# Performance work log

Hardware: AMD Instinct MI355X
Metric: run time of the kernel (lower is better)

## Reference

```python
import jax, jax.numpy as jnp
import numpy as np

START_TAG = 7
STOP_TAG = 8
NEG = -10000.0  # matches torch.full((1,K), -10000.) in the original


def setup_inputs() -> dict:
    key = jax.random.key(0)
    k1, k2, k3, k4 = jax.random.split(key, 4)
    B, T, K = 1024, 2048, 9  # K = output_dim + 2 (START/STOP hardcoded as 7/8)
    feats = jax.random.normal(k1, (B, T, K), dtype=jnp.float32)
    tags = jax.random.randint(k2, (B, T), 0, 7)            # valid labels 0..6
    lengths = jax.random.randint(k3, (B,), 1, T + 1)        # per-sentence lengths >= 1
    transitions = jax.random.normal(k4, (K, K), dtype=jnp.float32)
    transitions = transitions.at[START_TAG, :].set(NEG)     # never transition into START
    transitions = transitions.at[:, STOP_TAG].set(NEG)      # never transition out of STOP
    return {"feats": feats, "transitions": transitions, "tags": tags, "lengths": lengths}


def _crf_nll(feats, transitions, tags, lengths):
    # feats: [B,T,K] emissions, transitions[j,i] = score of i -> j
    B, T, K = feats.shape

    def fwd_one(feat, length):
        # CRF forward algorithm (log partition), vectorized over tags,
        # lax.scan over time; masked past `length` to emulate feats[:x_len].
        alpha0 = jnp.full((K,), NEG, feat.dtype).at[START_TAG].set(0.0)

        def step(alpha, inp):
            t, f = inp
            # alpha_new[j] = logsumexp_i(alpha[i] + transitions[j,i]) + feat[t,j]
            new = jax.nn.logsumexp(alpha[None, :] + transitions, axis=1) + f
            return jnp.where(t < length, new, alpha), None

        alpha, _ = jax.lax.scan(step, alpha0, (jnp.arange(T), feat))
        return jax.nn.logsumexp(alpha + transitions[STOP_TAG])

    fwd_scores = jax.vmap(fwd_one)(feats, lengths)  # [B]

    def gold_one(feat, tg, length):
        # _score_sentence: sum_t trans[tags[t], tags[t-1]] + feat[t, tags[t]]
        prev = jnp.concatenate([jnp.array([START_TAG], tg.dtype), tg[:-1]])
        step_scores = transitions[tg, prev] + jnp.take_along_axis(feat, tg[:, None], axis=1)[:, 0]
        mask = jnp.arange(tg.shape[0]) < length
        last = tg[length - 1]
        return jnp.sum(jnp.where(mask, step_scores, 0.0)) + transitions[STOP_TAG, last]

    gold_scores = jax.vmap(gold_one)(feats, tags, lengths)  # [B]

    # neg_log_likelihood accumulates (forward - gold) per sentence, then / n
    return jnp.mean(fwd_scores - gold_scores)


def reference(feats, transitions, tags, lengths):
    return _crf_nll(feats, transitions, tags, lengths)
```

## Files before the change

kernel.cpp:

```cpp
#include <hip/hip_runtime.h>


#define START_TAG 7
#define STOP_TAG  8
#define KDIM      9
#define NS        7
#define CHUNKS    32
#define NEGINF    (-1e30f)

__device__ __forceinline__ float rfl(float x) {
    return __int_as_float(__builtin_amdgcn_readfirstlane(__float_as_int(x)));
}

__global__ __launch_bounds__(256) void crf_fused_kernel(
    const float* __restrict__ feats,
    const float* __restrict__ trans,
    const int*   __restrict__ tags,
    const int*   __restrict__ lengths,
    float* __restrict__ out,
    int B, int T, int L)
{
    __shared__ float s_trans[81];
    __shared__ float s_E[49];
    __shared__ float s_M[CHUNKS * 64];
    __shared__ float s_gold[4];

    const int tid = threadIdx.x;
    const int b   = blockIdx.x;

    if (tid < 81) s_trans[tid] = trans[tid];
    if (tid >= 128 && tid < 177) {
        int k = tid - 128;
        s_E[k] = __expf(trans[(k / 7) * 9 + (k % 7)]);
    }
    __syncthreads();

    const int    len   = lengths[b];
    const int*   tg    = tags  + (size_t)b * T;
    const float* fbase = feats + (size_t)b * T * KDIM;

    {
        int per = (T >> 8) > 0 ? (T >> 8) : 1;
        int t0  = tid * per;
        float g = 0.f;
        if (t0 < len) {
            int te   = min(t0 + per, len);
            int prev = (t0 == 0) ? START_TAG : tg[t0 - 1];
            if (per == 8) {
                #pragma unroll
                for (int k = 0; k < 8; ++k) {
                    int t   = t0 + k;
                    int tc  = min(t, te - 1);
                    int cur = tg[tc];
                    float v = s_trans[cur * 9 + prev] + fbase[(size_t)tc * KDIM + cur];
                    g += (t < te) ? v : 0.f;
                    prev = cur;
                }
            } else {
                for (int k = 0; k < per; ++k) {
                    int t   = t0 + k;
                    int tc  = min(t, te - 1);
                    int cur = tg[tc];
                    float v = s_trans[cur * 9 + prev] + fbase[(size_t)tc * KDIM + cur];
                    g += (t < te) ? v : 0.f;
                    prev = cur;
                }
            }
            if (len - 1 >= t0 && len - 1 < t0 + per)
                g += s_trans[STOP_TAG * 9 + tg[len - 1]];
        }
        #pragma unroll
        for (int off = 32; off > 0; off >>= 1) g += __shfl_xor(g, off, 64);
        if ((tid & 63) == 0) s_gold[tid >> 6] = g;
    }

    {
        const int lane8  = tid & 7;
        const int c      = tid >> 3;
        const int t0     = c * L;
        const int tstart = max(t0, 1);
        const int tend   = min(t0 + L, len);

        if (lane8 < NS) {
            float* Mw = s_M + c * 64;
            if (tstart < tend) {
                float E[49];
                #pragma unroll
                for (int k = 0; k < 49; ++k) E[k] = rfl(s_E[k]);

                int baddr[NS];
                #pragma unroll
                for (int j = 0; j < NS; ++j) baddr[j] = (((tid & 56) | j) << 2);

                float p[NS];
                #pragma unroll
                for (int j = 0; j < NS; ++j) p[j] = (j == lane8) ? 1.f : 0.f;
                float s = 0.f;
                int rem = tend - tstart;

                const float* fp = fbase + (size_t)tstart * KDIM + lane8;

                #define CRF_STEP(XF) do {                                       \
                    float q[NS];                                                \
                    _Pragma("unroll")                                           \
                    for (int j = 0; j < NS; ++j) {                              \
                        float acc = E[j * 7] * p[0];                            \
                        _Pragma("unroll")                                       \
                        for (int i = 1; i < NS; ++i)                            \
                            acc = fmaf(E[j * 7 + i], p[i], acc);                \
                        q[j] = acc;                                             \
                    }                                                           \
                    float myef = __expf(XF);                                    \
                    _Pragma("unroll")                                           \
                    for (int j = 0; j < NS; ++j) {                              \
                        float efj = __int_as_float(                             \
                            __builtin_amdgcn_ds_bpermute(                       \
                                baddr[j], __float_as_int(myef)));               \
                        p[j] = q[j] * efj;                                      \
                    }                                                           \
                } while (0)

                #define CRF_RENORM() do {                                       \
                    float m = p[0];                                             \
                    _Pragma("unroll")                                           \
                    for (int j = 1; j < NS; ++j) m = fmaxf(m, p[j]);            \
                    float rm = __builtin_amdgcn_rcpf(m);                        \
                    _Pragma("unroll")                                           \
                    for (int j = 0; j < NS; ++j) p[j] *= rm;                    \
                    s += __logf(m);                                             \
                } while (0)

                int o1 = KDIM * min(1, rem - 1);
                int o2 = KDIM * min(2, rem - 1);
                int o3 = KDIM * min(3, rem - 1);
                float x0 = fp[0], x1 = fp[o1], x2 = fp[o2], x3 = fp[o3];
                fp += 4 * KDIM;

                while (rem >= 8) {
                    float y0 = fp[0], y1 = fp[KDIM], y2 = fp[2 * KDIM], y3 = fp[3 * KDIM];
                    fp += 4 * KDIM;
                    CRF_STEP(x0); CRF_STEP(x1); CRF_STEP(x2); CRF_STEP(x3);
                    CRF_RENORM();
                    x0 = y0; x1 = y1; x2 = y2; x3 = y3;
                    rem -= 4;
                }
                if (rem > 4) {
                    int e1 = KDIM * min(1, rem - 5);
                    int e2 = KDIM * min(2, rem - 5);
                    float y0 = fp[0], y1 = fp[e1], y2 = fp[e2];
                    CRF_STEP(x0); CRF_STEP(x1); CRF_STEP(x2); CRF_STEP(x3);
                    CRF_RENORM();
                    x0 = y0; x1 = y1; x2 = y2;
                    rem -= 4;
                }
                CRF_STEP(x0);
                if (rem > 1) CRF_STEP(x1);
                if (rem > 2) CRF_STEP(x2);
                if (rem > 3) CRF_STEP(x3);

                #pragma unroll
                for (int j = 0; j < NS; ++j)
                    Mw[j * 8 + lane8] = __logf(p[j]) + s;
                #undef CRF_STEP
                #undef CRF_RENORM
            } else {
                #pragma unroll
                for (int j = 0; j < NS; ++j)
                    Mw[j * 8 + lane8] = (j == lane8) ? 0.f : NEGINF;
            }
        }
    }
    __syncthreads();

    if (tid < 8) {
        const int  lane  = tid;
        const bool isrow = (lane < NS);
        const int  row   = isrow ? lane : 0;

        float a, S;
        {
            float a0 = isrow ? (s_trans[lane * 9 + START_TAG] + fbase[lane]) : NEGINF;
            float m = a0;
            #pragma unroll
            for (int off = 4; off > 0; off >>= 1) m = fmaxf(m, __shfl_xor(m, off, 8));
            a = a0 - m;
            S = m;
        }

        const int nc = min(CHUNKS, (len + L - 1) / L);
        const float* Mr0 = s_M + row * 8;
        float4 mA = *(const float4*)(Mr0);
        float4 mB = *(const float4*)(Mr0 + 4);
        for (int c = 0; c < nc; ++c) {
            int cn = min(c + 1, CHUNKS - 1);
            float4 nA = *(const float4*)(Mr0 + cn * 64);
            float4 nB = *(const float4*)(Mr0 + cn * 64 + 4);
            float tv[NS] = { mA.x, mA.y, mA.z, mA.w, mB.x, mB.y, mB.z };
            float tm = NEGINF;
            #pragma unroll
            for (int i = 0; i < NS; ++i) {
                tv[i] += __shfl(a, i, 8);
                tm = fmaxf(tm, tv[i]);
            }
            float sum = 0.f;
            #pragma unroll
            for (int i = 0; i < NS; ++i) sum += __expf(tv[i] - tm);
            float na = isrow ? (tm + __logf(sum)) : NEGINF;
            float m2 = na;
            #pragma unroll
            for (int off = 4; off > 0; off >>= 1) m2 = fmaxf(m2, __shfl_xor(m2, off, 8));
            a = na - m2;
            S += m2;
            mA = nA; mB = nB;
        }

        float term = isrow ? (a + s_trans[STOP_TAG * 9 + lane]) : NEGINF;
        float tm2 = term;
        #pragma unroll
        for (int off = 4; off > 0; off >>= 1) tm2 = fmaxf(tm2, __shfl_xor(tm2, off, 8));
        float e = isrow ? __expf(term - tm2) : 0.f;
        #pragma unroll
        for (int off = 4; off > 0; off >>= 1) e += __shfl_xor(e, off, 8);

        if (lane == 0) {
            float fwd = S + tm2 + __logf(e);
            float g = s_gold[0] + s_gold[1] + s_gold[2] + s_gold[3];
            atomicAdd(out, (fwd - g) * (1.0f / (float)B));
        }
    }
}

__global__ void init_out_kernel(float* out) {
    if (threadIdx.x == 0) out[0] = 0.f;
}

extern "C" void kernel_launch(void* const* d_in, const int* in_sizes, int n_in,
                              void* d_out, int out_size, void* d_ws, size_t ws_size,
                              hipStream_t stream) {
    const float* feats   = (const float*)d_in[0];
    const float* trans   = (const float*)d_in[1];
    const int*   tags    = (const int*)d_in[2];
    const int*   lengths = (const int*)d_in[3];

    int B = in_sizes[3];
    int T = in_sizes[2] / B;
    int L = (T + CHUNKS - 1) / CHUNKS;

    init_out_kernel<<<1, 64, 0, stream>>>((float*)d_out);
    crf_fused_kernel<<<B, 256, 0, stream>>>(
        feats, trans, tags, lengths, (float*)d_out, B, T, L);
}
```

Before: 157.3 us.

## Size chunks by per-sentence length and batch emission broadcasts ahead of matmuls

Chunk length is now derived from each sentence's actual length rather than the padded T, so all 32 chunks share the real work evenly instead of idle chunks past the length. The four ds_bpermute broadcasts per unrolled group are issued before the four matrix steps, which lets the cross-lane latency overlap with the multiply work. The serial combine over chunks keeps the full 7-vector in every lane, replacing the shuffle-based max and sum reductions with local arithmetic plus seven broadcasts. This raises register pressure, and the per-block chunk count now varies with length.

```diff
diff --git a/kernel.cpp b/kernel.cpp
--- a/kernel.cpp
+++ b/kernel.cpp
@@ -18,7 +18,7 @@
     const int*   __restrict__ tags,
     const int*   __restrict__ lengths,
     float* __restrict__ out,
-    int B, int T, int L)
+    int B, int T)
 {
     __shared__ float s_trans[81];
     __shared__ float s_E[49];
@@ -38,6 +38,7 @@
     const int    len   = lengths[b];
     const int*   tg    = tags  + (size_t)b * T;
     const float* fbase = feats + (size_t)b * T * KDIM;
+    const int    Lb    = (len > 1) ? ((len - 1 + CHUNKS - 1) / CHUNKS) : 1;
 
     {
         int per = (T >> 8) > 0 ? (T >> 8) : 1;
@@ -77,9 +78,8 @@
     {
         const int lane8  = tid & 7;
         const int c      = tid >> 3;
-        const int t0     = c * L;
-        const int tstart = max(t0, 1);
-        const int tend   = min(t0 + L, len);
+        const int tstart = 1 + c * Lb;
+        const int tend   = min(tstart + Lb, len);
 
         if (lane8 < NS) {
             float* Mw = s_M + c * 64;
@@ -100,7 +100,7 @@
 
                 const float* fp = fbase + (size_t)tstart * KDIM + lane8;
 
-                #define CRF_STEP(XF) do {                                       \
+                #define CRF_MAT(EF) do {                                        \
                     float q[NS];                                                \
                     _Pragma("unroll")                                           \
                     for (int j = 0; j < NS; ++j) {                              \
@@ -110,14 +110,23 @@
                             acc = fmaf(E[j * 7 + i], p[i], acc);                \
                         q[j] = acc;                                             \
                     }                                                           \
-                    float myef = __expf(XF);                                    \
-                    _Pragma("unroll")                                           \
-                    for (int j = 0; j < NS; ++j) {                              \
-                        float efj = __int_as_float(                             \
+                    _Pragma("unroll")                                           \
+                    for (int j = 0; j < NS; ++j) p[j] = q[j] * EF[j];           \
+                } while (0)
+
+                #define CRF_BCAST(DST, XF) do {                                 \
+                    float _e = __expf(XF);                                      \
+                    _Pragma("unroll")                                           \
+                    for (int j = 0; j < NS; ++j)                                \
+                        DST[j] = __int_as_float(                                \
                             __builtin_amdgcn_ds_bpermute(                       \
-                                baddr[j], __float_as_int(myef)));               \
-                        p[j] = q[j] * efj;                                      \
-                    }                                                           \
+                                baddr[j], __float_as_int(_e)));                 \
+                } while (0)
+
+                #define CRF_STEP(XF) do {                                       \
+                    float _ef[NS];                                              \
+                    CRF_BCAST(_ef, XF);                                         \
+                    CRF_MAT(_ef);                                               \
                 } while (0)
 
                 #define CRF_RENORM() do {                                       \
@@ -139,7 +148,12 @@
                 while (rem >= 8) {
                     float y0 = fp[0], y1 = fp[KDIM], y2 = fp[2 * KDIM], y3 = fp[3 * KDIM];
                     fp += 4 * KDIM;
-                    CRF_STEP(x0); CRF_STEP(x1); CRF_STEP(x2); CRF_STEP(x3);
+                    float efA[NS], efB[NS], efC[NS], efD[NS];
+                    CRF_BCAST(efA, x0);
+                    CRF_BCAST(efB, x1);
+                    CRF_BCAST(efC, x2);
+                    CRF_BCAST(efD, x3);
+                    CRF_MAT(efA); CRF_MAT(efB); CRF_MAT(efC); CRF_MAT(efD);
                     CRF_RENORM();
                     x0 = y0; x1 = y1; x2 = y2; x3 = y3;
                     rem -= 4;
@@ -148,7 +162,12 @@
                     int e1 = KDIM * min(1, rem - 5);
                     int e2 = KDIM * min(2, rem - 5);
                     float y0 = fp[0], y1 = fp[e1], y2 = fp[e2];
-                    CRF_STEP(x0); CRF_STEP(x1); CRF_STEP(x2); CRF_STEP(x3);
+                    float efA[NS], efB[NS], efC[NS], efD[NS];
+                    CRF_BCAST(efA, x0);
+                    CRF_BCAST(efB, x1);
+                    CRF_BCAST(efC, x2);
+                    CRF_BCAST(efD, x3);
+                    CRF_MAT(efA); CRF_MAT(efB); CRF_MAT(efC); CRF_MAT(efD);
                     CRF_RENORM();
                     x0 = y0; x1 = y1; x2 = y2;
                     rem -= 4;
@@ -161,6 +180,9 @@
                 #pragma unroll
                 for (int j = 0; j < NS; ++j)
                     Mw[j * 8 + lane8] = __logf(p[j]) + s;
+
+                #undef CRF_MAT
+                #undef CRF_BCAST
                 #undef CRF_STEP
                 #undef CRF_RENORM
             } else {
@@ -177,53 +199,65 @@
         const bool isrow = (lane < NS);
         const int  row   = isrow ? lane : 0;
 
-        float a, S;
+        float a[NS];
+        #pragma unroll
+        for (int i = 0; i < NS; ++i)
+            a[i] = s_trans[i * 9 + START_TAG] + fbase[i];
+        float S;
         {
-            float a0 = isrow ? (s_trans[lane * 9 + START_TAG] + fbase[lane]) : NEGINF;
-            float m = a0;
+            float mm = fmaxf(fmaxf(fmaxf(a[0], a[1]), fmaxf(a[2], a[3])),
+                             fmaxf(fmaxf(a[4], a[5]), a[6]));
+            S = mm;
             #pragma unroll
-            for (int off = 4; off > 0; off >>= 1) m = fmaxf(m, __shfl_xor(m, off, 8));
-            a = a0 - m;
-            S = m;
-        }
-
-        const int nc = min(CHUNKS, (len + L - 1) / L);
+            for (int i = 0; i < NS; ++i) a[i] -= mm;
+        }
+
+        int nc = (len > 1) ? ((len - 1 + Lb - 1) / Lb) : 0;
+        if (nc > CHUNKS) nc = CHUNKS;
+
         const float* Mr0 = s_M + row * 8;
         float4 mA = *(const float4*)(Mr0);
         float4 mB = *(const float4*)(Mr0 + 4);
-        for (int c = 0; c < nc; ++c) {
-            int cn = min(c + 1, CHUNKS - 1);
+        for (int cc = 0; cc < nc; ++cc) {
+            int cn = min(cc + 1, CHUNKS - 1);
             float4 nA = *(const float4*)(Mr0 + cn * 64);
             float4 nB = *(const float4*)(Mr0 + cn * 64 + 4);
-            float tv[NS] = { mA.x, mA.y, mA.z, mA.w, mB.x, mB.y, mB.z };
-            float tm = NEGINF;
-            #pragma unroll
-            for (int i = 0; i < NS; ++i) {
-                tv[i] += __shfl(a, i, 8);
-                tm = fmaxf(tm, tv[i]);
-            }
-            float sum = 0.f;
-            #pragma unroll
-            for (int i = 0; i < NS; ++i) sum += __expf(tv[i] - tm);
-            float na = isrow ? (tm + __logf(sum)) : NEGINF;
-            float m2 = na;
-            #pragma unroll
-            for (int off = 4; off > 0; off >>= 1) m2 = fmaxf(m2, __shfl_xor(m2, off, 8));
-            a = na - m2;
-            S += m2;
+            float t0 = mA.x + a[0], t1 = mA.y + a[1], t2 = mA.z + a[2];
+            float t3 = mA.w + a[3], t4 = mB.x + a[4], t5 = mB.y + a[5];
+            float t6 = mB.z + a[6];
+            float tm = fmaxf(fmaxf(fmaxf(t0, t1), fmaxf(t2, t3)),
+                             fmaxf(fmaxf(t4, t5), t6));
+            float e0 = __expf(t0 - tm), e1 = __expf(t1 - tm), e2 = __expf(t2 - tm);
+            float e3 = __expf(t3 - tm), e4 = __expf(t4 - tm), e5 = __expf(t5 - tm);
+            float e6 = __expf(t6 - tm);
+            float sum = ((e0 + e1) + (e2 + e3)) + ((e4 + e5) + e6);
+            float na = tm + __logf(sum);
+            float b0 = __shfl(na, 0, 8), b1 = __shfl(na, 1, 8), b2 = __shfl(na, 2, 8);
+            float b3 = __shfl(na, 3, 8), b4 = __shfl(na, 4, 8), b5 = __shfl(na, 5, 8);
+            float b6 = __shfl(na, 6, 8);
+            float mm = fmaxf(fmaxf(fmaxf(b0, b1), fmaxf(b2, b3)),
+                             fmaxf(fmaxf(b4, b5), b6));
+            a[0] = b0 - mm; a[1] = b1 - mm; a[2] = b2 - mm;
+            a[3] = b3 - mm; a[4] = b4 - mm; a[5] = b5 - mm;
+            a[6] = b6 - mm;
+            S += mm;
             mA = nA; mB = nB;
         }
 
-        float term = isrow ? (a + s_trans[STOP_TAG * 9 + lane]) : NEGINF;
-        float tm2 = term;
-        #pragma unroll
-        for (int off = 4; off > 0; off >>= 1) tm2 = fmaxf(tm2, __shfl_xor(tm2, off, 8));
-        float e = isrow ? __expf(term - tm2) : 0.f;
-        #pragma unroll
-        for (int off = 4; off > 0; off >>= 1) e += __shfl_xor(e, off, 8);
-
         if (lane == 0) {
-            float fwd = S + tm2 + __logf(e);
+            float t0 = a[0] + s_trans[STOP_TAG * 9 + 0];
+            float t1 = a[1] + s_trans[STOP_TAG * 9 + 1];
+            float t2 = a[2] + s_trans[STOP_TAG * 9 + 2];
+            float t3 = a[3] + s_trans[STOP_TAG * 9 + 3];
+            float t4 = a[4] + s_trans[STOP_TAG * 9 + 4];
+            float t5 = a[5] + s_trans[STOP_TAG * 9 + 5];
+            float t6 = a[6] + s_trans[STOP_TAG * 9 + 6];
+            float tm = fmaxf(fmaxf(fmaxf(t0, t1), fmaxf(t2, t3)),
+                             fmaxf(fmaxf(t4, t5), t6));
+            float sum = ((__expf(t0 - tm) + __expf(t1 - tm)) +
+                         (__expf(t2 - tm) + __expf(t3 - tm))) +
+                        ((__expf(t4 - tm) + __expf(t5 - tm)) + __expf(t6 - tm));
+            float fwd = S + tm + __logf(sum);
             float g = s_gold[0] + s_gold[1] + s_gold[2] + s_gold[3];
             atomicAdd(out, (fwd - g) * (1.0f / (float)B));
         }
@@ -244,9 +278,8 @@
 
     int B = in_sizes[3];
     int T = in_sizes[2] / B;
-    int L = (T + CHUNKS - 1) / CHUNKS;
 
     init_out_kernel<<<1, 64, 0, stream>>>((float*)d_out);
     crf_fused_kernel<<<B, 256, 0, stream>>>(
-        feats, trans, tags, lengths, (float*)d_out, B, T, L);
-}
+        feats, trans, tags, lengths, (float*)d_out, B, T);
+}
```

Result: no change. 154.5 us (-1.8%).
